# Performance work log

Measured on AMD Instinct MI355X. Metric: run time of the kernel, lower is better.

## Reference

```python
import jax, jax.numpy as jnp
import numpy as np
from jax import lax

B, C, H, W = 32, 512, 14, 14
NA = 9
N = H * W * NA  # 1764 anchors per image
IOU_THR = 0.3
SCORE_THR = 0.5
TOPK = 50


def setup_inputs() -> dict:
    key = jax.random.key(0)
    ks = jax.random.split(key, 8)
    def w(k, shape):
        return jax.random.normal(k, shape, jnp.float32) * 0.01  # nn.init.normal_(std=0.01)
    inp = {"features": jax.random.normal(ks[0], (B, C, H, W), jnp.float32)}
    # bbox head: 512->256 (GN32) ->128 (GN16) ->128 (GN16) -> 4*NA (1x1)
    inp["b1w"] = w(ks[1], (256, 512, 3, 3)); inp["b1b"] = jnp.zeros(256)
    inp["bg1w"] = jnp.ones(256); inp["bg1b"] = jnp.zeros(256)
    inp["b2w"] = w(ks[2], (128, 256, 3, 3)); inp["b2b"] = jnp.zeros(128)
    inp["bg2w"] = jnp.ones(128); inp["bg2b"] = jnp.zeros(128)
    inp["b3w"] = w(ks[3], (128, 128, 3, 3)); inp["b3b"] = jnp.zeros(128)
    inp["bg3w"] = jnp.ones(128); inp["bg3b"] = jnp.zeros(128)
    inp["b4w"] = w(ks[4], (4 * NA, 128, 1, 1)); inp["b4b"] = jnp.zeros(4 * NA)
    # classification head: 512->256 (GN32) ->128 (GN16) -> NA (1x1)
    inp["c1w"] = w(ks[5], (256, 512, 3, 3)); inp["c1b"] = jnp.zeros(256)
    inp["cg1w"] = jnp.ones(256); inp["cg1b"] = jnp.zeros(256)
    inp["c2w"] = w(ks[6], (128, 256, 3, 3)); inp["c2b"] = jnp.zeros(128)
    inp["cg2w"] = jnp.ones(128); inp["cg2b"] = jnp.zeros(128)
    inp["c3w"] = w(ks[7], (NA, 128, 1, 1)); inp["c3b"] = jnp.zeros(NA)
    return inp


def conv(x, w, b):
    k = w.shape[-1]
    pad = ((k // 2, k // 2), (k // 2, k // 2))
    y = lax.conv_general_dilated(x, w, (1, 1), pad, dimension_numbers=("NCHW", "OIHW", "NCHW"))
    return y + b[None, :, None, None]


def group_norm(x, w, b, groups, eps=1e-5):
    Bn, Cn, Hn, Wn = x.shape
    xg = x.reshape(Bn, groups, Cn // groups, Hn, Wn)
    mu = xg.mean(axis=(2, 3, 4), keepdims=True)
    var = xg.var(axis=(2, 3, 4), keepdims=True)
    xg = (xg - mu) * lax.rsqrt(var + eps)
    return xg.reshape(Bn, Cn, Hn, Wn) * w[None, :, None, None] + b[None, :, None, None]


def gelu(x):
    return jax.nn.gelu(x, approximate=False)  # torch nn.GELU default (erf)


def nms_single(boxes, scores):
    # boxes [N,4], scores [N]; greedy NMS, fixed-shape padded output [TOPK,5]
    valid = scores > SCORE_THR
    boxes = jnp.clip(boxes, 0.0, 1.0)
    order = jnp.argsort(-jnp.where(valid, scores, -jnp.inf))  # desc, invalid last
    b = boxes[order]; s = scores[order]; v = valid[order]
    x1 = jnp.maximum(b[:, None, 0], b[None, :, 0])
    y1 = jnp.maximum(b[:, None, 1], b[None, :, 1])
    x2 = jnp.minimum(b[:, None, 2], b[None, :, 2])
    y2 = jnp.minimum(b[:, None, 3], b[None, :, 3])
    inter = jnp.clip(x2 - x1, 0.0) * jnp.clip(y2 - y1, 0.0)
    area = (b[:, 2] - b[:, 0]) * (b[:, 3] - b[:, 1])
    iou = inter / (area[:, None] + area[None, :] - inter)
    # torch keeps when iou < thr; NaN compares False -> suppressed. Replicate exactly:
    suppress = jnp.logical_not(iou < IOU_THR)  # [N,N] bool
    idxs = jnp.arange(N)
    def body(suppressed, xs):
        row, i, vi = xs
        keep_i = vi & jnp.logical_not(suppressed[i])
        return suppressed | (keep_i & row & (idxs > i)), keep_i
    _, keep = lax.scan(body, jnp.zeros(N, bool), (suppress, idxs, v))
    kept_scores = jnp.where(keep, s, -1.0)
    topv, topi = lax.top_k(kept_scores, TOPK)  # first <=50 kept in score order
    out_boxes = jnp.where(topv[:, None] > 0.0, b[topi], 0.0)
    return jnp.concatenate([out_boxes, topv[:, None]], axis=-1)  # [TOPK, 5]; score=-1 marks pad


def _forward(features, b1w, b1b, bg1w, bg1b, b2w, b2b, bg2w, bg2b, b3w, b3b, bg3w, bg3b, b4w, b4b, c1w, c1b, cg1w, cg1b, c2w, c2b, cg2w, cg2b, c3w, c3b):
    bs = features.shape[0]
    h = group_norm(gelu(conv(features, b1w, b1b)), bg1w, bg1b, 32)
    h = group_norm(gelu(conv(h, b2w, b2b)), bg2w, bg2b, 16)
    h = group_norm(gelu(conv(h, b3w, b3b)), bg3w, bg3b, 16)
    bbox = conv(h, b4w, b4b).transpose(0, 2, 3, 1).reshape(bs, -1, 4)  # [B,N,4]
    h = group_norm(gelu(conv(features, c1w, c1b)), cg1w, cg1b, 32)
    h = group_norm(gelu(conv(h, c2w, c2b)), cg2w, cg2b, 16)
    conf = jax.nn.sigmoid(conv(h, c3w, c3b).transpose(0, 2, 3, 1).reshape(bs, -1))  # [B,N]
    return jax.vmap(nms_single)(bbox, conf)  # [B,TOPK,5]


def reference(features, b1w, b1b, bg1w, bg1b, b2w, b2b, bg2w, bg2b, b3w, b3b, bg3w, bg3b, b4w, b4b, c1w, c1b, cg1w, cg1b, c2w, c2b, cg2w, cg2b, c3w, c3b):
    return _forward(features, b1w, b1b, bg1w, bg1b, b2w, b2b, bg2w, bg2b, b3w, b3b, bg3w, bg3b, b4w, b4b, c1w, c1b, cg1w, cg1b, c2w, c2b, cg2w, cg2b, c3w, c3b)
```

## Files before the change

### kernel.cpp

```cpp
#include <hip/hip_runtime.h>
#include <hip/hip_bf16.h>
#include <math.h>

#define CHUNK 16
#define NN 1764
#define SORTN 2048

typedef float v2f __attribute__((ext_vector_type(2)));

__device__ inline void gl_lds16(const float* g, float* l) {
  __builtin_amdgcn_global_load_lds(
      (const __attribute__((address_space(1))) void*)g,
      (__attribute__((address_space(3))) void*)l, 16, 0, 0);
}

template<int Co, int Ci>
__device__ inline void seg_pack_pk(const float* __restrict__ src, float* __restrict__ dst, int i) {
  int co = i / (Ci * 9); int rem = i - co * (Ci * 9); int ci = rem / 9; int k = rem - ci * 9;
  int p = (co >> 5) * 16 + (co & 15);
  int h = (co & 31) >> 4;
  dst[((size_t)ci * (Co >> 1) + p) * 20 + 2 * k + h] = src[i];
}
template<int Co, int CiK>
__device__ inline void seg_tr(const float* __restrict__ src, float* __restrict__ dst, int i) {
  int co = i / CiK; int cik = i - co * CiK;
  dst[cik * Co + co] = src[i];
}

__device__ inline void seg_wino_u(const float* __restrict__ src, float* __restrict__ dst, int i) {
  int ci = i >> 8;
  int co = i & 255;
  const float* g = src + ((size_t)co * 512 + ci) * 9;
  float g00=g[0],g01=g[1],g02=g[2],g10=g[3],g11=g[4],g12=g[5],g20=g[6],g21=g[7],g22=g[8];
  float a[4][3];
  a[0][0]=g00; a[0][1]=g01; a[0][2]=g02;
  a[1][0]=0.5f*(g00+g10+g20); a[1][1]=0.5f*(g01+g11+g21); a[1][2]=0.5f*(g02+g12+g22);
  a[2][0]=0.5f*(g00-g10+g20); a[2][1]=0.5f*(g01-g11+g21); a[2][2]=0.5f*(g02-g12+g22);
  a[3][0]=g20; a[3][1]=g21; a[3][2]=g22;
  const int p_old = (co >> 5) * 16 + (co & 15);
  const int h = (co & 31) >> 4;
  const int pb = p_old >> 6, loc = p_old & 63;
  const int gg = loc >> 4, col = loc & 15;
  const int P = pb * 64 + (gg >> 1) * 32 + col * 2 + (gg & 1);
#pragma unroll
  for (int r4 = 0; r4 < 4; ++r4) {
    float u0 = a[r4][0];
    float u1 = 0.5f * (a[r4][0] + a[r4][1] + a[r4][2]);
    float u2 = 0.5f * (a[r4][0] - a[r4][1] + a[r4][2]);
    float u3 = a[r4][2];
    float uv[4] = {u0, u1, u2, u3};
#pragma unroll
    for (int c4 = 0; c4 < 4; ++c4) {
      int pos = r4 * 4 + c4;
      dst[(((size_t)pos * 512 + ci) * 128 + P) * 2 + h] = uv[c4];
    }
  }
}

__global__ void wtrans_wino_in(
  const float* __restrict__ b1w, const float* __restrict__ c1w,
  const float* __restrict__ b2w, const float* __restrict__ c2w,
  const float* __restrict__ b3w, const float* __restrict__ b4w,
  const float* __restrict__ c3w, const float* __restrict__ features,
  float* __restrict__ ub, float* __restrict__ uc,
  float* __restrict__ wp2b, float* __restrict__ wp2c,
  float* __restrict__ wp3b, float* __restrict__ wt4b, float* __restrict__ wt3c,
  float* __restrict__ V)
{
  const int bx = blockIdx.x;
  if (bx < 3927) {
    int j = bx * 256 + threadIdx.x;
    if (j < 131072) { seg_wino_u(b1w, ub, j); return; } j -= 131072;
    if (j < 131072) { seg_wino_u(c1w, uc, j); return; } j -= 131072;
    if (j < 294912) { seg_pack_pk<128, 256>(b2w, wp2b, j); return; } j -= 294912;
    if (j < 294912) { seg_pack_pk<128, 256>(c2w, wp2c, j); return; } j -= 294912;
    if (j < 147456) { seg_pack_pk<128, 128>(b3w, wp3b, j); return; } j -= 147456;
    if (j < 4608)   { seg_tr<36, 128>(b4w, wt4b, j); return; }  j -= 4608;
    if (j < 1152)   { seg_tr<9, 128>(c3w, wt3c, j); return; }
    return;
  }
  const int idx = bx - 3927;
  const int b = idx >> 7, cig = idx & 127;
  const int tid = threadIdx.x;
  if (tid >= 196) return;
  const int ci = cig * 4 + tid / 49;
  const int t  = tid % 49;
  const int ty = t / 7, tx = t % 7;
  const float* fp = features + ((size_t)b * 512 + ci) * 196;
  const int y0 = 2 * ty - 1, x0 = 2 * tx - 1;
  float d[4][4];
#pragma unroll
  for (int i = 0; i < 4; ++i) {
    const int y = y0 + i;
#pragma unroll
    for (int j = 0; j < 4; ++j) {
      const int x = x0 + j;
      d[i][j] = (y >= 0 && y < 14 && x >= 0 && x < 14) ? fp[y * 14 + x] : 0.0f;
    }
  }
  float tr[4][4];
#pragma unroll
  for (int j = 0; j < 4; ++j) {
    tr[0][j] = d[0][j] - d[2][j];
    tr[1][j] = d[1][j] + d[2][j];
    tr[2][j] = d[2][j] - d[1][j];
    tr[3][j] = d[1][j] - d[3][j];
  }
  const size_t m = (size_t)b * 49 + t;
#pragma unroll
  for (int i = 0; i < 4; ++i) {
    float v0 = tr[i][0] - tr[i][2];
    float v1 = tr[i][1] + tr[i][2];
    float v2 = tr[i][2] - tr[i][1];
    float v3 = tr[i][1] - tr[i][3];
    V[((size_t)(i * 4 + 0) * 512 + ci) * 1568 + m] = v0;
    V[((size_t)(i * 4 + 1) * 512 + ci) * 1568 + m] = v1;
    V[((size_t)(i * 4 + 2) * 512 + ci) * 1568 + m] = v2;
    V[((size_t)(i * 4 + 3) * 512 + ci) * 1568 + m] = v3;
  }
}

__global__ __launch_bounds__(256, 2) void wino_gemm(
    const float* __restrict__ V, const float* __restrict__ U, float* __restrict__ M)
{
  const int pos = blockIdx.x;
  const int mb  = blockIdx.y;
  const int q   = blockIdx.z;
  const int head = q >> 1;
  const int pb   = q & 1;
  const int tid = threadIdx.x;
  const int col = tid & 15;
  const int r   = tid >> 4;
  const int wv  = tid >> 6;

  __shared__ float vbuf[2][16][64];
  __shared__ float ubuf[2][16][128];

  const float* Uh = U + (size_t)head * 2097152;
  float* Mh = M + (size_t)head * 6422528;
  const int m0 = mb * 64;

  const float* vg  = V + ((size_t)pos * 512 + (tid >> 4)) * 1568 + m0 + (tid & 15) * 4;
  const int c1 = 256 + tid;
  const float* ug0 = Uh + ((size_t)pos * 512 + (tid >> 5)) * 256 + pb * 128 + (tid & 31) * 4;
  const float* ug1 = Uh + ((size_t)pos * 512 + (c1 >> 5)) * 256 + pb * 128 + (c1 & 31) * 4;
  float* vls = ((float*)vbuf) + wv * 256;
  float* uls = ((float*)ubuf) + wv * 256;

  gl_lds16(vg, vls);
  gl_lds16(ug0, uls);
  gl_lds16(ug1, uls + 1024);
  __syncthreads();

  v2f acc[4][4];
#pragma unroll
  for (int g = 0; g < 4; ++g)
#pragma unroll
    for (int j = 0; j < 4; ++j) acc[g][j] = (v2f)(0.0f);

  int cur = 0;
  for (int cb = 0; cb < 32; ++cb) {
    if (cb + 1 < 32) {
      const int nb = cur ^ 1;
      gl_lds16(vg + (size_t)(cb + 1) * 16 * 1568, vls + nb * 1024);
      gl_lds16(ug0 + (size_t)(cb + 1) * 16 * 256, uls + nb * 2048);
      gl_lds16(ug1 + (size_t)(cb + 1) * 16 * 256, uls + nb * 2048 + 1024);
    }
#pragma unroll
    for (int ci = 0; ci < 16; ++ci) {
      const float4* uq0 = (const float4*)&ubuf[cur][ci][col * 4];
      const float4* uq1 = (const float4*)&ubuf[cur][ci][64 + col * 4];
      float4 a = uq0[0], bq = uq1[0];
      v2f u2[4] = { (v2f){a.x, a.y}, (v2f){a.z, a.w},
                    (v2f){bq.x, bq.y}, (v2f){bq.z, bq.w} };
      const float4* vp = (const float4*)&vbuf[cur][ci][r * 4];
      float4 v0 = vp[0];
      float vv[4] = {v0.x, v0.y, v0.z, v0.w};
#pragma unroll
      for (int j = 0; j < 4; ++j) {
        v2f s2 = (v2f){vv[j], vv[j]};
#pragma unroll
        for (int g = 0; g < 4; ++g)
          acc[g][j] = __builtin_elementwise_fma(u2[g], s2, acc[g][j]);
      }
    }
    __syncthreads();
    cur ^= 1;
  }

  const int mm = m0 + r * 4;
  if (mm < 1568) {
#pragma unroll
    for (int g = 0; g < 4; ++g) {
      const int p = pb * 64 + g * 16 + col;
      const int cox = (p >> 4) * 32 + (p & 15);
      float* ox = Mh + ((size_t)pos * 256 + cox) * 1568 + mm;
      float* oy = ox + (size_t)16 * 1568;
#pragma unroll
      for (int j = 0; j < 4; ++j) { ox[j] = acc[g][j].x; oy[j] = acc[g][j].y; }
    }
  }
}

__global__ __launch_bounds__(256) void wino_out_gn(
    const float* __restrict__ M,
    const float* __restrict__ bsb, const float* __restrict__ bsc,
    const float* __restrict__ gwb, const float* __restrict__ gwc,
    const float* __restrict__ gbb, const float* __restrict__ gbc,
    float* __restrict__ outb, float* __restrict__ outc)
{
  const int bx = blockIdx.x;
  const int b  = blockIdx.y;
  const int head = bx >> 4, cog = bx & 15;
  const int tid = threadIdx.x;
  const float* Mh = M + (size_t)head * 6422528;
  const float* bs = head ? bsc : bsb;
  const float* gw = head ? gwc : gwb;
  const float* gb = head ? gbc : gbb;
  float* out      = head ? outc : outb;
  const int co0 = cog * 16;

  __shared__ float red[4][4];
  __shared__ float stats[4];

  const bool pa = tid < 196;
  const int csub = tid / 49;
  const int t    = tid % 49;
  const int ty = t / 7, tx = t % 7;
  const size_t mt = (size_t)b * 49 + t;

  float y4[4][4];
  float s = 0.f, q = 0.f;
  if (pa) {
#pragma unroll
    for (int cc = 0; cc < 4; ++cc) {
      const int co = co0 + csub * 4 + cc;
      const float* mp = Mh + (size_t)co * 1568 + mt;
      float m16[16];
#pragma unroll
      for (int pos = 0; pos < 16; ++pos)
        m16[pos] = mp[(size_t)pos * 401408];
      float Z0[4], Z1[4];
#pragma unroll
      for (int j = 0; j < 4; ++j) {
        Z0[j] = m16[0 * 4 + j] + m16[1 * 4 + j] + m16[2 * 4 + j];
        Z1[j] = m16[1 * 4 + j] - m16[2 * 4 + j] - m16[3 * 4 + j];
      }
      const float bias = bs[co];
      float yv[4];
      yv[0] = Z0[0] + Z0[1] + Z0[2];
      yv[1] = Z0[1] - Z0[2] - Z0[3];
      yv[2] = Z1[0] + Z1[1] + Z1[2];
      yv[3] = Z1[1] - Z1[2] - Z1[3];
#pragma unroll
      for (int k = 0; k < 4; ++k) {
        float x = yv[k] + bias;
        float g = 0.5f * x * (1.0f + erff(x * 0.70710678118654752440f));
        y4[cc][k] = g;
        s += g; q += g * g;
      }
    }
  }
  float s0 = (pa && csub < 2) ? s : 0.f, q0 = (pa && csub < 2) ? q : 0.f;
  float s1 = (pa && csub >= 2) ? s : 0.f, q1 = (pa && csub >= 2) ? q : 0.f;
#pragma unroll
  for (int off = 32; off > 0; off >>= 1) {
    s0 += __shfl_down(s0, off, 64); q0 += __shfl_down(q0, off, 64);
    s1 += __shfl_down(s1, off, 64); q1 += __shfl_down(q1, off, 64);
  }
  const int wave = tid >> 6, lane = tid & 63;
  if (lane == 0) { red[wave][0] = s0; red[wave][1] = q0; red[wave][2] = s1; red[wave][3] = q1; }
  __syncthreads();
  if (tid == 0) {
    float S0 = red[0][0] + red[1][0] + red[2][0] + red[3][0];
    float Q0 = red[0][1] + red[1][1] + red[2][1] + red[3][1];
    float S1 = red[0][2] + red[1][2] + red[2][2] + red[3][2];
    float Q1 = red[0][3] + red[1][3] + red[2][3] + red[3][3];
    float m0 = S0 * (1.0f / 1568.0f);
    float v0 = Q0 * (1.0f / 1568.0f) - m0 * m0;
    float m1 = S1 * (1.0f / 1568.0f);
    float v1 = Q1 * (1.0f / 1568.0f) - m1 * m1;
    stats[0] = m0; stats[1] = 1.0f / sqrtf(v0 + 1e-5f);
    stats[2] = m1; stats[3] = 1.0f / sqrtf(v1 + 1e-5f);
  }
  __syncthreads();
  if (pa) {
    const float mg = (csub < 2) ? stats[0] : stats[2];
    const float iv = (csub < 2) ? stats[1] : stats[3];
#pragma unroll
    for (int cc = 0; cc < 4; ++cc) {
      const int co = co0 + csub * 4 + cc;
      const float w = gw[co], bb2 = gb[co];
      float* op = out + ((size_t)b * 256 + co) * 196;
#pragma unroll
      for (int dy = 0; dy < 2; ++dy)
#pragma unroll
        for (int dx = 0; dx < 2; ++dx) {
          float yv = (y4[cc][dy * 2 + dx] - mg) * iv * w + bb2;
          op[(2 * ty + dy) * 14 + (2 * tx + dx)] = yv;
        }
    }
  }
}

template<int COPT>
__global__ __launch_bounds__(256, 2) void conv3x3_part(
    const float* __restrict__ in0, const float* __restrict__ in1,
    const float* __restrict__ wt0, const float* __restrict__ wt1,
    float* __restrict__ po0, float* __restrict__ po1,
    int Cin, int Cout, int cobPerHead, int cinPerSplit, size_t sStride)
{
  constexpr int NP = COPT / 2;
  constexpr int NPP = 16 * NP;
  constexpr int NPAIR = 8 * NPP;
  const int tid = threadIdx.x;
  const int bx  = blockIdx.x;
  const int b   = blockIdx.y;
  const int s   = blockIdx.z;
  const int head = bx / cobPerHead;
  const int cob  = bx - head * cobPerHead;
  const float* in  = head ? in1  : in0;
  const float* wt  = head ? wt1  : wt0;
  float* po        = head ? po1  : po0;
  const int co0 = cob * (16 * COPT);

  const int col = tid & 15;
  const int r   = tid >> 4;
  const bool ract = r < 14;

  __shared__ float tile[2][CHUNK][16][16];
  __shared__ float wbuf[2][8][NPP][20];

  {
    float* tz = &tile[0][0][0][0];
    for (int i = tid; i < 2 * CHUNK * 256; i += 256) tz[i] = 0.0f;
  }
  __syncthreads();

  const int p = tid;
  const bool pa = p < 196;
  const int prow = p / 14, pcol = p - prow * 14;
  const float* inb = in + (size_t)b * Cin * 196;
  const int cb0 = (s * cinPerSplit) / CHUNK;
  const int nch = cinPerSplit / CHUNK;
  const int CoutH = Cout >> 1;

  const int sciL = tid / NPP;
  const int spp  = tid - sciL * NPP;
  const bool sact = tid < NPAIR;
  const int spidx = ((co0 >> 5) + (spp >> 4)) * 16 + (spp & 15);

  if (pa) {
#pragma unroll
    for (int ci = 0; ci < CHUNK; ++ci)
      tile[0][ci][prow + 1][pcol + 1] = inb[(cb0 * CHUNK + ci) * 196 + p];
  }
  if (sact) {
    const float4* src = (const float4*)(wt + ((size_t)(cb0 * CHUNK + sciL) * CoutH + spidx) * 20);
    float4 q0 = src[0], q1 = src[1], q2 = src[2], q3 = src[3], q4 = src[4];
    float4* dst = (float4*)&wbuf[0][sciL][spp][0];
    dst[0] = q0; dst[1] = q1; dst[2] = q2; dst[3] = q3; dst[4] = q4;
  }
  __syncthreads();

  v2f acc[NP][14];
#pragma unroll
  for (int g = 0; g < NP; ++g)
#pragma unroll
    for (int j = 0; j < 14; ++j) acc[g][j] = (v2f)(0.0f);

  int wcur = 0;
  for (int lcb = 0; lcb < nch; ++lcb) {
    const int cbg = cb0 + lcb;
    const int cur = lcb & 1;
    const bool more = (lcb + 1 < nch);
    float v[CHUNK];
    if (more && pa) {
#pragma unroll
      for (int ci = 0; ci < CHUNK; ++ci)
        v[ci] = inb[((cbg + 1) * CHUNK + ci) * 196 + p];
    }
#pragma unroll
    for (int half = 0; half < 2; ++half) {
      const bool hasNext = (half == 0) || more;
      const int nbase = (half == 0) ? (cbg * CHUNK + 8) : ((cbg + 1) * CHUNK);
      float4 q0, q1, q2, q3, q4;
      if (hasNext && sact) {
        const float4* src = (const float4*)(wt + ((size_t)(nbase + sciL) * CoutH + spidx) * 20);
        q0 = src[0]; q1 = src[1]; q2 = src[2]; q3 = src[3]; q4 = src[4];
      }
      if (ract) {
#pragma unroll
        for (int ciL = 0; ciL < 8; ++ciL) {
          const int ci = half * 8 + ciL;
          v2f w2[NP][9];
#pragma unroll
          for (int g = 0; g < NP; ++g) {
            const float4* wq = (const float4*)&wbuf[wcur][ciL][g * 16 + col][0];
            float4 a0 = wq[0], a1 = wq[1], a2 = wq[2], a3 = wq[3], a4 = wq[4];
            w2[g][0] = (v2f){a0.x, a0.y}; w2[g][1] = (v2f){a0.z, a0.w};
            w2[g][2] = (v2f){a1.x, a1.y}; w2[g][3] = (v2f){a1.z, a1.w};
            w2[g][4] = (v2f){a2.x, a2.y}; w2[g][5] = (v2f){a2.z, a2.w};
            w2[g][6] = (v2f){a3.x, a3.y}; w2[g][7] = (v2f){a3.z, a3.w};
            w2[g][8] = (v2f){a4.x, a4.y};
          }
          float nb[3][16];
#pragma unroll
          for (int dr = 0; dr < 3; ++dr) {
            const float4* rp = (const float4*)(&tile[cur][ci][r + dr][0]);
            float4 a = rp[0], bq = rp[1], cq = rp[2], dq = rp[3];
            nb[dr][0]  = a.x;  nb[dr][1]  = a.y;  nb[dr][2]  = a.z;  nb[dr][3]  = a.w;
            nb[dr][4]  = bq.x; nb[dr][5]  = bq.y; nb[dr][6]  = bq.z; nb[dr][7]  = bq.w;
            nb[dr][8]  = cq.x; nb[dr][9]  = cq.y; nb[dr][10] = cq.z; nb[dr][11] = cq.w;
            nb[dr][12] = dq.x; nb[dr][13] = dq.y; nb[dr][14] = dq.z; nb[dr][15] = dq.w;
          }
#pragma unroll
          for (int ky = 0; ky < 3; ++ky)
#pragma unroll
            for (int kx = 0; kx < 3; ++kx) {
#pragma unroll
              for (int g = 0; g < NP; ++g) {
                v2f w = w2[g][ky * 3 + kx];
#pragma unroll
                for (int j = 0; j < 14; ++j) {
                  float s_ = nb[ky][j + kx];
                  v2f nbv = (v2f){s_, s_};
                  acc[g][j] = __builtin_elementwise_fma(w, nbv, acc[g][j]);
                }
              }
            }
        }
      }
      if (hasNext && sact) {
        float4* dst = (float4*)&wbuf[wcur ^ 1][sciL][spp][0];
        dst[0] = q0; dst[1] = q1; dst[2] = q2; dst[3] = q3; dst[4] = q4;
      }
      if (half == 1 && more && pa) {
#pragma unroll
        for (int ci = 0; ci < CHUNK; ++ci)
          tile[1 - cur][ci][prow + 1][pcol + 1] = v[ci];
      }
      __syncthreads();
      wcur ^= 1;
    }
  }

  if (ract) {
#pragma unroll
    for (int g = 0; g < NP; ++g) {
      const int ocx = 32 * g + col;
      const int ocy = ocx + 16;
      float* opx = po + (size_t)s * sStride + ((size_t)b * Cout + co0 + ocx) * 196 + r * 14;
      float* opy = po + (size_t)s * sStride + ((size_t)b * Cout + co0 + ocy) * 196 + r * 14;
#pragma unroll
      for (int j = 0; j < 14; ++j) { opx[j] = acc[g][j].x; opy[j] = acc[g][j].y; }
    }
  }
}

template<int S>
__global__ __launch_bounds__(256) void combine_gn(
    const float* __restrict__ po0, const float* __restrict__ po1,
    const float* __restrict__ bs0, const float* __restrict__ bs1,
    const float* __restrict__ gw0, const float* __restrict__ gw1,
    const float* __restrict__ gb0, const float* __restrict__ gb1,
    float* __restrict__ out0, float* __restrict__ out1,
    int Cout, int cobPerHead, size_t sStride)
{
  const int tid = threadIdx.x, bx = blockIdx.x, b = blockIdx.y;
  const int head = bx / cobPerHead, cob = bx - head * cobPerHead;
  const float* po = head ? po1 : po0;
  const float* bs = head ? bs1 : bs0;
  const float* gw = head ? gw1 : gw0;
  const float* gb = head ? gb1 : gb0;
  float* out      = head ? out1 : out0;
  const int co0 = cob * 16;

  __shared__ float red[4][4];
  __shared__ float stats[4];

  const int p = tid;
  const bool pa = p < 196;
  float v[16];
  float s0 = 0.f, q0 = 0.f, s1 = 0.f, q1 = 0.f;
  if (pa) {
#pragma unroll
    for (int c = 0; c < 16; ++c) {
      const size_t base = ((size_t)b * Cout + co0 + c) * 196 + p;
      float x = bs[co0 + c];
#pragma unroll
      for (int s = 0; s < S; ++s) x += po[base + (size_t)s * sStride];
      float g = 0.5f * x * (1.0f + erff(x * 0.70710678118654752440f));
      v[c] = g;
      if (c < 8) { s0 += g; q0 += g * g; } else { s1 += g; q1 += g * g; }
    }
  }
#pragma unroll
  for (int off = 32; off > 0; off >>= 1) {
    s0 += __shfl_down(s0, off, 64); q0 += __shfl_down(q0, off, 64);
    s1 += __shfl_down(s1, off, 64); q1 += __shfl_down(q1, off, 64);
  }
  const int wave = tid >> 6, lane = tid & 63;
  if (lane == 0) { red[wave][0] = s0; red[wave][1] = q0; red[wave][2] = s1; red[wave][3] = q1; }
  __syncthreads();
  if (tid == 0) {
    float S0 = red[0][0] + red[1][0] + red[2][0] + red[3][0];
    float Q0 = red[0][1] + red[1][1] + red[2][1] + red[3][1];
    float S1 = red[0][2] + red[1][2] + red[2][2] + red[3][2];
    float Q1 = red[0][3] + red[1][3] + red[2][3] + red[3][3];
    float m0 = S0 * (1.0f / 1568.0f);
    float v0 = Q0 * (1.0f / 1568.0f) - m0 * m0;
    float m1 = S1 * (1.0f / 1568.0f);
    float v1 = Q1 * (1.0f / 1568.0f) - m1 * m1;
    stats[0] = m0; stats[1] = 1.0f / sqrtf(v0 + 1e-5f);
    stats[2] = m1; stats[3] = 1.0f / sqrtf(v1 + 1e-5f);
  }
  __syncthreads();
  if (pa) {
    float m0 = stats[0], i0 = stats[1], m1 = stats[2], i1 = stats[3];
#pragma unroll
    for (int c = 0; c < 16; ++c) {
      float m  = (c < 8) ? m0 : m1;
      float iv = (c < 8) ? i0 : i1;
      float y = (v[c] - m) * iv * gw[co0 + c] + gb[co0 + c];
      out[((size_t)b * Cout + co0 + c) * 196 + p] = y;
    }
  }
}

__global__ __launch_bounds__(512) void nms_kernel(
  const float* __restrict__ tb, const float* __restrict__ tc,
  const float* __restrict__ wtb, const float* __restrict__ wtc,
  const float* __restrict__ bb,  const float* __restrict__ bc,
  float* __restrict__ bbox, float* __restrict__ out)
{
  const int b = blockIdx.x, tid = threadIdx.x;
  __shared__ unsigned long long key[SORTN];
  __shared__ float sx1[NN], sy1[NN], sx2[NN], sy2[NN], sar[NN], ssc[NN];
  __shared__ unsigned char sup[NN];
  __shared__ int sV, sMin;

  if (tid == 0) sV = 0;
  for (int i = NN + tid; i < SORTN; i += 512) key[i] = 0ull;

  int cntv = 0;
  if (tid < 196) {
    const int p = tid;
    float ab[36], ac[9];
#pragma unroll
    for (int o = 0; o < 36; ++o) ab[o] = bb[o];
#pragma unroll
    for (int o = 0; o < 9; ++o)  ac[o] = bc[o];
    const float* pb = tb + (size_t)b * 128 * 196 + p;
    const float* pc = tc + (size_t)b * 128 * 196 + p;
    for (int ci = 0; ci < 128; ++ci) {
      float xb = pb[ci * 196];
      float xc = pc[ci * 196];
      const float* wB = wtb + ci * 36;
      const float* wC = wtc + ci * 9;
#pragma unroll
      for (int o = 0; o < 36; ++o) ab[o] = fmaf(wB[o], xb, ab[o]);
#pragma unroll
      for (int o = 0; o < 9; ++o)  ac[o] = fmaf(wC[o], xc, ac[o]);
    }
    float* bp = bbox + ((size_t)b * NN) * 4 + (size_t)p * 36;
#pragma unroll
    for (int o = 0; o < 36; ++o) bp[o] = ab[o];
#pragma unroll
    for (int a = 0; a < 9; ++a) {
      float s = 1.0f / (1.0f + expf(-ac[a]));
      const int n = p * 9 + a;
      unsigned rank = (unsigned)(NN - 1 - n);
      unsigned long long k;
      if (s > 0.5f) { k = (((unsigned long long)__float_as_uint(s)) << 32) | rank; cntv++; }
      else k = (unsigned long long)rank;
      key[n] = k;
    }
  }
  atomicAdd(&sV, cntv);
  __syncthreads();
  const int V = sV;

  for (int kk = 2; kk <= SORTN; kk <<= 1) {
    for (int j = kk >> 1; j > 0; j >>= 1) {
      for (int i = tid; i < SORTN; i += 512) {
        int ixj = i ^ j;
        if (ixj > i) {
          unsigned long long a = key[i], c = key[ixj];
          bool dirDesc = ((i & kk) == 0);
          if ((a < c) == dirDesc) { key[i] = c; key[ixj] = a; }
        }
      }
      __syncthreads();
    }
  }

  const float* bbb = bbox + (size_t)b * NN * 4;
  for (int i = tid; i < V; i += 512) {
    unsigned long long k = key[i];
    int idx = NN - 1 - (int)(unsigned)(k & 0xFFFFFFFFull);
    float s = __uint_as_float((unsigned)(k >> 32));
    const float* bp = bbb + (size_t)idx * 4;
    float x1 = fminf(fmaxf(bp[0], 0.0f), 1.0f);
    float y1 = fminf(fmaxf(bp[1], 0.0f), 1.0f);
    float x2 = fminf(fmaxf(bp[2], 0.0f), 1.0f);
    float y2 = fminf(fmaxf(bp[3], 0.0f), 1.0f);
    sx1[i] = x1; sy1[i] = y1; sx2[i] = x2; sy2[i] = y2;
    sar[i] = (x2 - x1) * (y2 - y1);
    ssc[i] = s;
    sup[i] = 0;
  }
  __syncthreads();

  int kept = 0, cur = 0;
  float* ob = out + (size_t)b * 50 * 5;
  while (kept < 50 && cur < V) {
    int nxt = -1;
    for (int base = cur; base < V; base += 512) {
      if (tid == 0) sMin = 0x7FFFFFFF;
      __syncthreads();
      int i = base + tid;
      if (i < V && !sup[i]) atomicMin(&sMin, i);
      __syncthreads();
      if (sMin != 0x7FFFFFFF) { nxt = sMin; break; }
    }
    if (nxt < 0) break;
    float kx1 = sx1[nxt], ky1 = sy1[nxt], kx2 = sx2[nxt], ky2 = sy2[nxt], ka = sar[nxt];
    if (tid == 0) {
      float* rr = ob + kept * 5;
      rr[0] = kx1; rr[1] = ky1; rr[2] = kx2; rr[3] = ky2; rr[4] = ssc[nxt];
    }
    kept++;
    for (int jj = nxt + 1 + tid; jj < V; jj += 512) {
      if (!sup[jj]) {
        float xx1 = fmaxf(kx1, sx1[jj]);
        float yy1 = fmaxf(ky1, sy1[jj]);
        float xx2 = fminf(kx2, sx2[jj]);
        float yy2 = fminf(ky2, sy2[jj]);
        float inter = fmaxf(xx2 - xx1, 0.0f) * fmaxf(yy2 - yy1, 0.0f);
        float iou = inter / ((ka + sar[jj]) - inter);
        if (!(iou < 0.3f)) sup[jj] = 1;
      }
    }
    cur = nxt + 1;
    __syncthreads();
  }
  for (int rr = kept + tid; rr < 50; rr += 512) {
    float* qq = ob + rr * 5;
    qq[0] = 0.0f; qq[1] = 0.0f; qq[2] = 0.0f; qq[3] = 0.0f; qq[4] = -1.0f;
  }
}

extern "C" void kernel_launch(void* const* d_in, const int* in_sizes, int n_in,
                              void* d_out, int out_size, void* d_ws, size_t ws_size,
                              hipStream_t stream)
{
  const float* features = (const float*)d_in[0];
  const float* b1w = (const float*)d_in[1];  const float* b1b = (const float*)d_in[2];
  const float* bg1w = (const float*)d_in[3]; const float* bg1b = (const float*)d_in[4];
  const float* b2w = (const float*)d_in[5];  const float* b2b = (const float*)d_in[6];
  const float* bg2w = (const float*)d_in[7]; const float* bg2b = (const float*)d_in[8];
  const float* b3w = (const float*)d_in[9];  const float* b3b = (const float*)d_in[10];
  const float* bg3w = (const float*)d_in[11]; const float* bg3b = (const float*)d_in[12];
  const float* b4w = (const float*)d_in[13]; const float* b4b = (const float*)d_in[14];
  const float* c1w = (const float*)d_in[15]; const float* c1b = (const float*)d_in[16];
  const float* cg1w = (const float*)d_in[17]; const float* cg1b = (const float*)d_in[18];
  const float* c2w = (const float*)d_in[19]; const float* c2b = (const float*)d_in[20];
  const float* cg2w = (const float*)d_in[21]; const float* cg2b = (const float*)d_in[22];
  const float* c3w = (const float*)d_in[23]; const float* c3b = (const float*)d_in[24];

  float* ws = (float*)d_ws;
  float* U    = ws; ws += 4194304;
  float* wp2b = ws; ws += 327680;
  float* wp2c = ws; ws += 327680;
  float* wp3b = ws; ws += 163840;
  float* wt4b = ws; ws += 4608;
  float* wt3c = ws; ws += 1152;
  float* t1b  = ws; ws += 1605632;
  float* t1c  = ws; ws += 1605632;
  float* t2b  = ws; ws += 802816;
  float* t2c  = ws; ws += 802816;
  float* V    = ws; ws += 12845056;
  float* M    = ws; ws += 12845056;
  float* bbox = ws; ws += 225792;
  float* P    = V;
  float* t3b  = t1b;

  wtrans_wino_in<<<8023, 256, 0, stream>>>(b1w, c1w, b2w, c2w, b3w, b4w, c3w,
                                           features,
                                           U, U + 2097152, wp2b, wp2c, wp3b,
                                           wt4b, wt3c, V);

  wino_gemm<<<dim3(16, 25, 4), 256, 0, stream>>>(V, U, M);
  wino_out_gn<<<dim3(32, 32), 256, 0, stream>>>(M, b1b, c1b, bg1w, cg1w, bg1b, cg1b, t1b, t1c);

  {
    const size_t sStr = (size_t)32 * 128 * 196;
    conv3x3_part<4><<<dim3(4, 32, 4), 256, 0, stream>>>(
        t1b, t1c, wp2b, wp2c, P, P + 4 * sStr, 256, 128, 2, 64, sStr);
    combine_gn<4><<<dim3(16, 32), 256, 0, stream>>>(
        P, P + 4 * sStr, b2b, c2b, bg2w, cg2w, bg2b, cg2b, t2b, t2c, 128, 8, sStr);
  }
  {
    const size_t sStr = (size_t)32 * 128 * 196;
    conv3x3_part<2><<<dim3(4, 32, 4), 256, 0, stream>>>(
        t2b, t2b, wp3b, wp3b, P, P, 128, 128, 4, 32, sStr);
    combine_gn<4><<<dim3(8, 32), 256, 0, stream>>>(
        P, P, b3b, b3b, bg3w, bg3w, bg3b, bg3b, t3b, t3b, 128, 8, sStr);
  }

  nms_kernel<<<32, 512, 0, stream>>>(t3b, t2c, wt4b, wt3c, b4b, c3b, bbox, (float*)d_out);
}
```

Before: 650.4 us.

## Use Winograd F(2,3) for second conv layer, fusing input transform into GN epilogue

The second 3x3 conv of both heads (256->128) now uses Winograd F(2x2,3x3) instead of direct convolution with split-K partials. The layer-1 GroupNorm epilogue stages normalized output in LDS and writes the Winograd input transform V directly, skipping the t1 intermediate. A new GEMM kernel and an output-transform+GELU+GN kernel replace conv3x3_part and combine_gn. This cuts multiply count and the partial-sum combine pass, at the cost of extra 16x-expanded V/M traffic and a larger shared-memory footprint in the fused kernel.

After: 628.3 us. 3.4% less time.

```diff
diff --git a/kernel.cpp b/kernel.cpp
--- a/kernel.cpp
+++ b/kernel.cpp
@@ -57,29 +57,58 @@
   }
 }
 
+__device__ inline void seg_wino_u2(const float* __restrict__ src, float* __restrict__ dst, int i) {
+  int ci = i >> 7;
+  int co = i & 127;
+  const float* g = src + ((size_t)co * 256 + ci) * 9;
+  float g00=g[0],g01=g[1],g02=g[2],g10=g[3],g11=g[4],g12=g[5],g20=g[6],g21=g[7],g22=g[8];
+  float a[4][3];
+  a[0][0]=g00; a[0][1]=g01; a[0][2]=g02;
+  a[1][0]=0.5f*(g00+g10+g20); a[1][1]=0.5f*(g01+g11+g21); a[1][2]=0.5f*(g02+g12+g22);
+  a[2][0]=0.5f*(g00-g10+g20); a[2][1]=0.5f*(g01-g11+g21); a[2][2]=0.5f*(g02-g12+g22);
+  a[3][0]=g20; a[3][1]=g21; a[3][2]=g22;
+  const int p_old = (co >> 5) * 16 + (co & 15);
+  const int h = (co & 31) >> 4;
+  const int gg = p_old >> 4, col = p_old & 15;
+  const int P = (gg >> 1) * 32 + col * 2 + (gg & 1);
+#pragma unroll
+  for (int r4 = 0; r4 < 4; ++r4) {
+    float u0 = a[r4][0];
+    float u1 = 0.5f * (a[r4][0] + a[r4][1] + a[r4][2]);
+    float u2 = 0.5f * (a[r4][0] - a[r4][1] + a[r4][2]);
+    float u3 = a[r4][2];
+    float uv[4] = {u0, u1, u2, u3};
+#pragma unroll
+    for (int c4 = 0; c4 < 4; ++c4) {
+      int pos = r4 * 4 + c4;
+      dst[(((size_t)pos * 256 + ci) * 64 + P) * 2 + h] = uv[c4];
+    }
+  }
+}
+
 __global__ void wtrans_wino_in(
   const float* __restrict__ b1w, const float* __restrict__ c1w,
   const float* __restrict__ b2w, const float* __restrict__ c2w,
   const float* __restrict__ b3w, const float* __restrict__ b4w,
   const float* __restrict__ c3w, const float* __restrict__ features,
   float* __restrict__ ub, float* __restrict__ uc,
-  float* __restrict__ wp2b, float* __restrict__ wp2c,
+  float* __restrict__ u2b, float* __restrict__ u2c,
   float* __restrict__ wp3b, float* __restrict__ wt4b, float* __restrict__ wt3c,
   float* __restrict__ V)
 {
   const int bx = blockIdx.x;
-  if (bx < 3927) {
+  if (bx < 1879) {
     int j = bx * 256 + threadIdx.x;
     if (j < 131072) { seg_wino_u(b1w, ub, j); return; } j -= 131072;
     if (j < 131072) { seg_wino_u(c1w, uc, j); return; } j -= 131072;
-    if (j < 294912) { seg_pack_pk<128, 256>(b2w, wp2b, j); return; } j -= 294912;
-    if (j < 294912) { seg_pack_pk<128, 256>(c2w, wp2c, j); return; } j -= 294912;
+    if (j < 32768)  { seg_wino_u2(b2w, u2b, j); return; } j -= 32768;
+    if (j < 32768)  { seg_wino_u2(c2w, u2c, j); return; } j -= 32768;
     if (j < 147456) { seg_pack_pk<128, 128>(b3w, wp3b, j); return; } j -= 147456;
     if (j < 4608)   { seg_tr<36, 128>(b4w, wt4b, j); return; }  j -= 4608;
     if (j < 1152)   { seg_tr<9, 128>(c3w, wt3c, j); return; }
     return;
   }
-  const int idx = bx - 3927;
+  const int idx = bx - 1879;
   const int b = idx >> 7, cig = idx & 127;
   const int tid = threadIdx.x;
   if (tid >= 196) return;
@@ -202,12 +231,92 @@
   }
 }
 
-__global__ __launch_bounds__(256) void wino_out_gn(
+__global__ __launch_bounds__(256, 2) void wino_gemm2(
+    const float* __restrict__ V2, const float* __restrict__ U2, float* __restrict__ M2)
+{
+  const int pos = blockIdx.x;
+  const int mb  = blockIdx.y;
+  const int head = blockIdx.z;
+  const int tid = threadIdx.x;
+  const int col = tid & 15;
+  const int r   = tid >> 4;
+  const int wv  = tid >> 6;
+
+  __shared__ float vbuf[2][16][64];
+  __shared__ float ubuf[2][16][128];
+
+  const float* Vh = V2 + (size_t)head * 6422528;
+  const float* Uh = U2 + (size_t)head * 524288;
+  float* Mh = M2 + (size_t)head * 3211264;
+  const int m0 = mb * 64;
+
+  const float* vg  = Vh + ((size_t)pos * 256 + (tid >> 4)) * 1568 + m0 + (tid & 15) * 4;
+  const float* ug0 = Uh + ((size_t)pos * 256 + (tid >> 5)) * 128 + (tid & 31) * 4;
+  const float* ug1 = Uh + ((size_t)pos * 256 + 8 + (tid >> 5)) * 128 + (tid & 31) * 4;
+  float* vls = ((float*)vbuf) + wv * 256;
+  float* uls = ((float*)ubuf) + wv * 256;
+
+  gl_lds16(vg, vls);
+  gl_lds16(ug0, uls);
+  gl_lds16(ug1, uls + 1024);
+  __syncthreads();
+
+  v2f acc[4][4];
+#pragma unroll
+  for (int g = 0; g < 4; ++g)
+#pragma unroll
+    for (int j = 0; j < 4; ++j) acc[g][j] = (v2f)(0.0f);
+
+  int cur = 0;
+  for (int cb = 0; cb < 16; ++cb) {
+    if (cb + 1 < 16) {
+      const int nb = cur ^ 1;
+      gl_lds16(vg + (size_t)(cb + 1) * 16 * 1568, vls + nb * 1024);
+      gl_lds16(ug0 + (size_t)(cb + 1) * 16 * 128, uls + nb * 2048);
+      gl_lds16(ug1 + (size_t)(cb + 1) * 16 * 128, uls + nb * 2048 + 1024);
+    }
+#pragma unroll
+    for (int ci = 0; ci < 16; ++ci) {
+      const float4* uq0 = (const float4*)&ubuf[cur][ci][col * 4];
+      const float4* uq1 = (const float4*)&ubuf[cur][ci][64 + col * 4];
+      float4 a = uq0[0], bq = uq1[0];
+      v2f u2[4] = { (v2f){a.x, a.y}, (v2f){a.z, a.w},
+                    (v2f){bq.x, bq.y}, (v2f){bq.z, bq.w} };
+      const float4* vp = (const float4*)&vbuf[cur][ci][r * 4];
+      float4 v0 = vp[0];
+      float vv[4] = {v0.x, v0.y, v0.z, v0.w};
+#pragma unroll
+      for (int j = 0; j < 4; ++j) {
+        v2f s2 = (v2f){vv[j], vv[j]};
+#pragma unroll
+        for (int g = 0; g < 4; ++g)
+          acc[g][j] = __builtin_elementwise_fma(u2[g], s2, acc[g][j]);
+      }
+    }
+    __syncthreads();
+    cur ^= 1;
+  }
+
+  const int mm = m0 + r * 4;
+  if (mm < 1568) {
+#pragma unroll
+    for (int g = 0; g < 4; ++g) {
+      const int p = g * 16 + col;
+      const int cox = (p >> 4) * 32 + (p & 15);
+      float* ox = Mh + ((size_t)pos * 128 + cox) * 1568 + mm;
+      float* oy = ox + (size_t)16 * 1568;
+#pragma unroll
+      for (int j = 0; j < 4; ++j) { ox[j] = acc[g][j].x; oy[j] = acc[g][j].y; }
+    }
+  }
+}
+
+__global__ __launch_bounds__(256) void wino_outin(
     const float* __restrict__ M,
     const float* __restrict__ bsb, const float* __restrict__ bsc,
     const float* __restrict__ gwb, const float* __restrict__ gwc,
     const float* __restrict__ gbb, const float* __restrict__ gbc,
-    float* __restrict__ outb, float* __restrict__ outc)
+    float* __restrict__ V2)
 {
   const int bx = blockIdx.x;
   const int b  = blockIdx.y;
@@ -217,11 +326,12 @@
   const float* bs = head ? bsc : bsb;
   const float* gw = head ? gwc : gwb;
   const float* gb = head ? gbc : gbb;
-  float* out      = head ? outc : outb;
+  float* Vh = V2 + (size_t)head * 6422528;
   const int co0 = cog * 16;
 
   __shared__ float red[4][4];
   __shared__ float stats[4];
+  __shared__ float ylds[16][196];
 
   const bool pa = tid < 196;
   const int csub = tid / 49;
@@ -291,7 +401,145 @@
     for (int cc = 0; cc < 4; ++cc) {
       const int co = co0 + csub * 4 + cc;
       const float w = gw[co], bb2 = gb[co];
-      float* op = out + ((size_t)b * 256 + co) * 196;
+#pragma unroll
+      for (int dy = 0; dy < 2; ++dy)
+#pragma unroll
+        for (int dx = 0; dx < 2; ++dx) {
+          float yv = (y4[cc][dy * 2 + dx] - mg) * iv * w + bb2;
+          ylds[csub * 4 + cc][(2 * ty + dy) * 14 + (2 * tx + dx)] = yv;
+        }
+    }
+  }
+  __syncthreads();
+  if (pa) {
+    const int y0 = 2 * ty - 1, x0 = 2 * tx - 1;
+#pragma unroll
+    for (int cc = 0; cc < 4; ++cc) {
+      const int cl = csub * 4 + cc;
+      const int ci2 = co0 + cl;
+      float d[4][4];
+#pragma unroll
+      for (int i = 0; i < 4; ++i) {
+        const int y = y0 + i;
+#pragma unroll
+        for (int j = 0; j < 4; ++j) {
+          const int x = x0 + j;
+          d[i][j] = (y >= 0 && y < 14 && x >= 0 && x < 14) ? ylds[cl][y * 14 + x] : 0.0f;
+        }
+      }
+      float tr[4][4];
+#pragma unroll
+      for (int j = 0; j < 4; ++j) {
+        tr[0][j] = d[0][j] - d[2][j];
+        tr[1][j] = d[1][j] + d[2][j];
+        tr[2][j] = d[2][j] - d[1][j];
+        tr[3][j] = d[1][j] - d[3][j];
+      }
+#pragma unroll
+      for (int i = 0; i < 4; ++i) {
+        float v0 = tr[i][0] - tr[i][2];
+        float v1 = tr[i][1] + tr[i][2];
+        float v2 = tr[i][2] - tr[i][1];
+        float v3 = tr[i][1] - tr[i][3];
+        Vh[((size_t)(i * 4 + 0) * 256 + ci2) * 1568 + mt] = v0;
+        Vh[((size_t)(i * 4 + 1) * 256 + ci2) * 1568 + mt] = v1;
+        Vh[((size_t)(i * 4 + 2) * 256 + ci2) * 1568 + mt] = v2;
+        Vh[((size_t)(i * 4 + 3) * 256 + ci2) * 1568 + mt] = v3;
+      }
+    }
+  }
+}
+
+__global__ __launch_bounds__(256) void wino_out_gn2(
+    const float* __restrict__ M2,
+    const float* __restrict__ bsb, const float* __restrict__ bsc,
+    const float* __restrict__ gwb, const float* __restrict__ gwc,
+    const float* __restrict__ gbb, const float* __restrict__ gbc,
+    float* __restrict__ outb, float* __restrict__ outc)
+{
+  const int bx = blockIdx.x;
+  const int b  = blockIdx.y;
+  const int head = bx >> 3, cog = bx & 7;
+  const int tid = threadIdx.x;
+  const float* Mh = M2 + (size_t)head * 3211264;
+  const float* bs = head ? bsc : bsb;
+  const float* gw = head ? gwc : gwb;
+  const float* gb = head ? gbc : gbb;
+  float* out      = head ? outc : outb;
+  const int co0 = cog * 16;
+
+  __shared__ float red[4][4];
+  __shared__ float stats[4];
+
+  const bool pa = tid < 196;
+  const int csub = tid / 49;
+  const int t    = tid % 49;
+  const int ty = t / 7, tx = t % 7;
+  const size_t mt = (size_t)b * 49 + t;
+
+  float y4[4][4];
+  float s = 0.f, q = 0.f;
+  if (pa) {
+#pragma unroll
+    for (int cc = 0; cc < 4; ++cc) {
+      const int co = co0 + csub * 4 + cc;
+      const float* mp = Mh + (size_t)co * 1568 + mt;
+      float m16[16];
+#pragma unroll
+      for (int pos = 0; pos < 16; ++pos)
+        m16[pos] = mp[(size_t)pos * 200704];
+      float Z0[4], Z1[4];
+#pragma unroll
+      for (int j = 0; j < 4; ++j) {
+        Z0[j] = m16[0 * 4 + j] + m16[1 * 4 + j] + m16[2 * 4 + j];
+        Z1[j] = m16[1 * 4 + j] - m16[2 * 4 + j] - m16[3 * 4 + j];
+      }
+      const float bias = bs[co];
+      float yv[4];
+      yv[0] = Z0[0] + Z0[1] + Z0[2];
+      yv[1] = Z0[1] - Z0[2] - Z0[3];
+      yv[2] = Z1[0] + Z1[1] + Z1[2];
+      yv[3] = Z1[1] - Z1[2] - Z1[3];
+#pragma unroll
+      for (int k = 0; k < 4; ++k) {
+        float x = yv[k] + bias;
+        float g = 0.5f * x * (1.0f + erff(x * 0.70710678118654752440f));
+        y4[cc][k] = g;
+        s += g; q += g * g;
+      }
+    }
+  }
+  float s0 = (pa && csub < 2) ? s : 0.f, q0 = (pa && csub < 2) ? q : 0.f;
+  float s1 = (pa && csub >= 2) ? s : 0.f, q1 = (pa && csub >= 2) ? q : 0.f;
+#pragma unroll
+  for (int off = 32; off > 0; off >>= 1) {
+    s0 += __shfl_down(s0, off, 64); q0 += __shfl_down(q0, off, 64);
+    s1 += __shfl_down(s1, off, 64); q1 += __shfl_down(q1, off, 64);
+  }
+  const int wave = tid >> 6, lane = tid & 63;
+  if (lane == 0) { red[wave][0] = s0; red[wave][1] = q0; red[wave][2] = s1; red[wave][3] = q1; }
+  __syncthreads();
+  if (tid == 0) {
+    float S0 = red[0][0] + red[1][0] + red[2][0] + red[3][0];
+    float Q0 = red[0][1] + red[1][1] + red[2][1] + red[3][1];
+    float S1 = red[0][2] + red[1][2] + red[2][2] + red[3][2];
+    float Q1 = red[0][3] + red[1][3] + red[2][3] + red[3][3];
+    float m0 = S0 * (1.0f / 1568.0f);
+    float v0 = Q0 * (1.0f / 1568.0f) - m0 * m0;
+    float m1 = S1 * (1.0f / 1568.0f);
+    float v1 = Q1 * (1.0f / 1568.0f) - m1 * m1;
+    stats[0] = m0; stats[1] = 1.0f / sqrtf(v0 + 1e-5f);
+    stats[2] = m1; stats[3] = 1.0f / sqrtf(v1 + 1e-5f);
+  }
+  __syncthreads();
+  if (pa) {
+    const float mg = (csub < 2) ? stats[0] : stats[2];
+    const float iv = (csub < 2) ? stats[1] : stats[3];
+#pragma unroll
+    for (int cc = 0; cc < 4; ++cc) {
+      const int co = co0 + csub * 4 + cc;
+      const float w = gw[co], bb2 = gb[co];
+      float* op = out + ((size_t)b * 128 + co) * 196;
 #pragma unroll
       for (int dy = 0; dy < 2; ++dy)
 #pragma unroll
@@ -671,43 +919,34 @@
 
   float* ws = (float*)d_ws;
   float* U    = ws; ws += 4194304;
-  float* wp2b = ws; ws += 327680;
-  float* wp2c = ws; ws += 327680;
+  float* U2   = ws; ws += 1048576;
   float* wp3b = ws; ws += 163840;
   float* wt4b = ws; ws += 4608;
   float* wt3c = ws; ws += 1152;
-  float* t1b  = ws; ws += 1605632;
-  float* t1c  = ws; ws += 1605632;
   float* t2b  = ws; ws += 802816;
   float* t2c  = ws; ws += 802816;
+  float* t3   = ws; ws += 802816;
   float* V    = ws; ws += 12845056;
   float* M    = ws; ws += 12845056;
   float* bbox = ws; ws += 225792;
   float* P    = V;
-  float* t3b  = t1b;
-
-  wtrans_wino_in<<<8023, 256, 0, stream>>>(b1w, c1w, b2w, c2w, b3w, b4w, c3w,
+
+  wtrans_wino_in<<<5975, 256, 0, stream>>>(b1w, c1w, b2w, c2w, b3w, b4w, c3w,
                                            features,
-                                           U, U + 2097152, wp2b, wp2c, wp3b,
-                                           wt4b, wt3c, V);
-
+                                           U, U + 2097152, U2, U2 + 524288,
+                                           wp3b, wt4b, wt3c, V);
   wino_gemm<<<dim3(16, 25, 4), 256, 0, stream>>>(V, U, M);
-  wino_out_gn<<<dim3(32, 32), 256, 0, stream>>>(M, b1b, c1b, bg1w, cg1w, bg1b, cg1b, t1b, t1c);
-
-  {
-    const size_t sStr = (size_t)32 * 128 * 196;
-    conv3x3_part<4><<<dim3(4, 32, 4), 256, 0, stream>>>(
-        t1b, t1c, wp2b, wp2c, P, P + 4 * sStr, 256, 128, 2, 64, sStr);
-    combine_gn<4><<<dim3(16, 32), 256, 0, stream>>>(
-        P, P + 4 * sStr, b2b, c2b, bg2w, cg2w, bg2b, cg2b, t2b, t2c, 128, 8, sStr);
-  }
+  wino_outin<<<dim3(32, 32), 256, 0, stream>>>(M, b1b, c1b, bg1w, cg1w, bg1b, cg1b, V);
+  wino_gemm2<<<dim3(16, 25, 2), 256, 0, stream>>>(V, U2, M);
+  wino_out_gn2<<<dim3(16, 32), 256, 0, stream>>>(M, b2b, c2b, bg2w, cg2w, bg2b, cg2b, t2b, t2c);
+
   {
     const size_t sStr = (size_t)32 * 128 * 196;
     conv3x3_part<2><<<dim3(4, 32, 4), 256, 0, stream>>>(
         t2b, t2b, wp3b, wp3b, P, P, 128, 128, 4, 32, sStr);
     combine_gn<4><<<dim3(8, 32), 256, 0, stream>>>(
-        P, P, b3b, b3b, bg3w, bg3w, bg3b, bg3b, t3b, t3b, 128, 8, sStr);
-  }
-
-  nms_kernel<<<32, 512, 0, stream>>>(t3b, t2c, wt4b, wt3c, b4b, c3b, bbox, (float*)d_out);
-}
+        P, P, b3b, b3b, bg3w, bg3w, bg3b, bg3b, t3, t3, 128, 8, sStr);
+  }
+
+  nms_kernel<<<32, 512, 0, stream>>>(t3, t2c, wt4b, wt3c, b4b, c3b, bbox, (float*)d_out);
+}
```
